# Kernel optimization log

Hardware: AMD Instinct MI355X
Metric: run time of the kernel (lower is better)

Reference implementation:

```python
import jax, jax.numpy as jnp
import numpy as np


def setup_inputs() -> dict:
    key = jax.random.key(0)
    ks = jax.random.split(key, 7)
    B, T, C, D = 8, 2048, 1024, 128
    x = jax.random.normal(ks[0], (B, T, C), dtype=jnp.float32)
    # torch nn.Linear weights are [out_features, in_features]
    s = 1.0 / np.sqrt(C)
    Wq = jax.random.normal(ks[1], (D, C), dtype=jnp.float32) * s
    bq = jax.random.normal(ks[2], (D,), dtype=jnp.float32) * s
    Wk = jax.random.normal(ks[3], (D, C), dtype=jnp.float32) * s
    bk = jax.random.normal(ks[4], (D,), dtype=jnp.float32) * s
    Wv = jax.random.normal(ks[5], (D, C), dtype=jnp.float32) * s
    bv = jax.random.normal(ks[6], (D,), dtype=jnp.float32) * s
    return {"x": x, "Wq": Wq, "bq": bq, "Wk": Wk, "bk": bk, "Wv": Wv, "bv": bv}


def reference(x, Wq, bq, Wk, bk, Wv, bv):
    B, T, C = x.shape
    q = jnp.einsum('btc,dc->btd', x, Wq) + bq  # [B,T,D]
    k = jnp.einsum('btc,dc->btd', x, Wk) + bk
    v = jnp.einsum('btc,dc->btd', x, Wv) + bv
    scores = jnp.einsum('btd,bsd->bts', q, k)  # [B,T,T]
    causal = jnp.tril(jnp.ones((T, T), dtype=bool))
    masked = jnp.where(causal, scores, -jnp.inf)
    # NOTE: original scales by sqrt(key.weight.shape[-1]) == sqrt(emb_dim), AFTER masking
    scale = jnp.asarray(C, dtype=x.dtype) ** 0.5
    attn = jax.nn.softmax(masked / scale, axis=-1)
    return jnp.einsum('bts,bsd->btd', attn, v)
```

## Files before the change

### kernel.cpp

```cpp
#include <hip/hip_runtime.h>
#include <hip/hip_bf16.h>
#include <math.h>

typedef __bf16 bf16_t;
typedef __bf16 bf16x4 __attribute__((ext_vector_type(4)));
typedef __bf16 bf16x8 __attribute__((ext_vector_type(8)));
typedef float  f32x4  __attribute__((ext_vector_type(4)));
typedef float  f32x16 __attribute__((ext_vector_type(16)));
typedef int    v2i    __attribute__((ext_vector_type(2)));

static constexpr int Bz = 8, Tt = 2048, Cc = 1024, Dd = 128;
static constexpr int Mm = Bz * Tt;
static constexpr int NT128 = Tt / 128;

__device__ __forceinline__ bf16x8 lds_read8(const char* base, int byte) {
    return *(const bf16x8*)(base + byte);
}

__device__ __forceinline__ bf16x8 cvt8(float4 a, float4 b) {
    bf16x8 r;
    r[0] = (bf16_t)a.x; r[1] = (bf16_t)a.y; r[2] = (bf16_t)a.z; r[3] = (bf16_t)a.w;
    r[4] = (bf16_t)b.x; r[5] = (bf16_t)b.y; r[6] = (bf16_t)b.z; r[7] = (bf16_t)b.w;
    return r;
}

__device__ __forceinline__ unsigned cvtpk(float lo, float hi) {
    unsigned r;
    asm("v_cvt_pk_bf16_f32 %0, %1, %2" : "=v"(r) : "v"(lo), "v"(hi));
    return r;
}

typedef const __attribute__((address_space(1))) unsigned int* as1_u32p;
typedef __attribute__((address_space(3))) unsigned int* as3_u32p;

__device__ __forceinline__ void gload_lds16(const bf16_t* g, bf16_t* l) {
    __builtin_amdgcn_global_load_lds((as1_u32p)(const void*)g, (as3_u32p)(void*)l, 16, 0, 0);
}

__global__ __launch_bounds__(256) void wcvt_kernel(
    const float* __restrict__ Wq, const float* __restrict__ Wk,
    const float* __restrict__ Wv, bf16_t* __restrict__ Wp)
{
    int g = (blockIdx.x * 256 + threadIdx.x) * 4;
    int n = g >> 10;
    int k = g & 1023;
    int sel = n >> 7;
    const float* W = (sel == 0) ? Wq : (sel == 1) ? Wk : Wv;
    float4 f = *(const float4*)(W + (size_t)(n & 127) * 1024 + k);
    bf16x4 o; o[0] = (bf16_t)f.x; o[1] = (bf16_t)f.y; o[2] = (bf16_t)f.z; o[3] = (bf16_t)f.w;
    int ktile = k >> 6, kk = (k >> 5) & 1, hi = (k >> 3) & 3, e = k & 7;
    int ng = n >> 4, cg = ng / 12, ngl = ng % 12, lo = n & 15;
    size_t addr = (size_t)(((((ktile * 2 + cg) * 12 + ngl) * 2 + kk) * 4 + hi) * 16 + lo) * 8 + e;
    *(bf16x4*)(Wp + addr) = o;
}

__global__ __launch_bounds__(512, 4) void qkv_fused(
    const float* __restrict__ x, const bf16_t* __restrict__ Wp,
    const float* __restrict__ bq, const float* __restrict__ bk, const float* __restrict__ bv,
    bf16_t* __restrict__ qo, bf16_t* __restrict__ ko, bf16_t* __restrict__ vTo)
{
    const int m0  = blockIdx.x * 64;
    const int cg  = blockIdx.y;
    const int tid = threadIdx.x;
    const int lane = tid & 63;
    const int wv  = tid >> 6;
    const int wr  = wv >> 2;
    const int cw  = wv & 3;
    const int lo  = lane & 15;
    const int hi  = lane >> 4;

    __shared__ bf16_t Wl[2][12 * 2 * 512];
    __shared__ bf16_t Xs[2][64 * 64];

    f32x4 zero4 = {0.f, 0.f, 0.f, 0.f};
    f32x4 acc[2][3];
    #pragma unroll
    for (int i = 0; i < 2; i++)
        #pragma unroll
        for (int j = 0; j < 3; j++) acc[i][j] = zero4;

    const int xrow = tid >> 3;
    const int xcol = (tid & 7) * 8;

    float4 fx[2];
    auto load_x = [&](int t) {
        const float4* s = (const float4*)(x + (size_t)(m0 + xrow) * Cc + t * 64 + xcol);
        fx[0] = s[0]; fx[1] = s[1];
    };
    auto write_x = [&](int buf) {
        int byte = (xrow * 128 + xcol * 2) ^ ((xrow & 7) << 4);
        *(bf16x8*)((char*)Xs[buf] + byte) = cvt8(fx[0], fx[1]);
    };
    auto stage_W = [&](int buf, int t) {
        const bf16_t* base = Wp + (size_t)(t * 2 + cg) * 12288;
        #pragma unroll
        for (int i = 0; i < 3; i++) {
            int c = i * 8 + wv;
            gload_lds16(base + c * 512 + lane * 8, Wl[buf] + c * 512);
        }
    };
    auto compute = [&](int buf) {
        #pragma unroll
        for (int kk = 0; kk < 2; kk++) {
            int r0 = wr * 32 + lo;
            int r1 = wr * 32 + 16 + lo;
            bf16x8 af0 = lds_read8((char*)Xs[buf], (r0 * 128 + kk * 64 + hi * 16) ^ ((r0 & 7) << 4));
            bf16x8 af1 = lds_read8((char*)Xs[buf], (r1 * 128 + kk * 64 + hi * 16) ^ ((r1 & 7) << 4));
            #pragma unroll
            for (int j = 0; j < 3; j++) {
                bf16x8 bf = *(const bf16x8*)(Wl[buf] + ((cw * 3 + j) * 2 + kk) * 512 + lane * 8);
                acc[0][j] = __builtin_amdgcn_mfma_f32_16x16x32_bf16(af0, bf, acc[0][j], 0, 0, 0);
                acc[1][j] = __builtin_amdgcn_mfma_f32_16x16x32_bf16(af1, bf, acc[1][j], 0, 0, 0);
            }
        }
    };

    load_x(0);
    stage_W(0, 0);
    write_x(0);
    load_x(1);
    asm volatile("s_waitcnt lgkmcnt(0)" ::: "memory");
    __builtin_amdgcn_s_barrier();

    #pragma unroll 1
    for (int t = 0; t < 16; t++) {
        const int buf = t & 1;
        if (t < 15) {
            stage_W(buf ^ 1, t + 1);
            asm volatile("s_waitcnt vmcnt(5)" ::: "memory");
        } else {
            asm volatile("s_waitcnt vmcnt(0)" ::: "memory");
        }
        __builtin_amdgcn_sched_barrier(0);
        compute(buf);
        if (t < 15) {
            write_x(buf ^ 1);
            if (t < 14) load_x(t + 2);
            asm volatile("s_waitcnt lgkmcnt(0)" ::: "memory");
            __builtin_amdgcn_s_barrier();
        }
    }

    #pragma unroll
    for (int j = 0; j < 3; j++) {
        int n = cg * 192 + cw * 48 + j * 16 + lo;
        int tsel = n >> 7, d = n & 127;
        const float* bp = (tsel == 0) ? bq : (tsel == 1) ? bk : bv;
        float bb = bp[d];
        #pragma unroll
        for (int i = 0; i < 2; i++)
            #pragma unroll
            for (int r = 0; r < 4; r++) {
                int m = m0 + wr * 32 + i * 16 + hi * 4 + r;
                float v = acc[i][j][r] + bb;
                if (tsel == 0)      qo[(size_t)m * Dd + d] = (bf16_t)v;
                else if (tsel == 1) ko[(size_t)m * Dd + d] = (bf16_t)v;
                else                vTo[(size_t)d * Mm + m] = (bf16_t)v;
            }
    }
}

__global__ __launch_bounds__(256, 2) void attn_kernel(
    const bf16_t* __restrict__ qi, const bf16_t* __restrict__ ki,
    const bf16_t* __restrict__ vTi,
    bf16_t* __restrict__ Opart, float* __restrict__ Mpart, float* __restrict__ Lpart,
    int nsplit)
{
    const int g   = blockIdx.x;
    const int per = nsplit * 8;
    const int qt  = (NT128 - 1) - g / per;
    const int rem = g % per;
    const int s   = rem >> 3;
    const int b   = rem & 7;
    const int nt  = 2 * qt + 2;
    const int t_lo = (s * nt) / nsplit;
    const int t_hi = ((s + 1) * nt) / nsplit;

    const int q0   = qt * 128;
    const int tid  = threadIdx.x;
    const int lane = tid & 63;
    const int w    = tid >> 6;
    const int rq   = lane & 31;
    const int dh   = lane >> 5;

    bf16_t* Ob = Opart + ((size_t)s * Mm + (size_t)b * Tt + q0) * Dd;
    float* Mb = Mpart + (size_t)s * Mm + (size_t)b * Tt + q0;
    float* Lb = Lpart + (size_t)s * Mm + (size_t)b * Tt + q0;

    if (t_lo >= t_hi) {
        float4 z = {0.f, 0.f, 0.f, 0.f};
        #pragma unroll
        for (int i = 0; i < 8; i++)
            ((float4*)Ob)[i * 256 + tid] = z;
        if (tid < 128) { Mb[tid] = -INFINITY; Lb[tid] = 0.f; }
        return;
    }

    __shared__ __align__(16) char smem[65536];

    const float SCALE = 1.4426950408889634f / 32.0f;
    const int qg = q0 + w * 32 + rq;
    const int qwmax = q0 + w * 32 + 31;

    bf16x8 qf[8];
    {
        const bf16_t* qrow = qi + (size_t)(b * Tt + qg) * Dd;
        #pragma unroll
        for (int ks = 0; ks < 8; ks++)
            qf[ks] = *(const bf16x8*)(qrow + ks * 16 + dh * 8);
    }

    f32x16 accO[4];
    #pragma unroll
    for (int ds = 0; ds < 4; ds++)
        #pragma unroll
        for (int e = 0; e < 16; e++) accO[ds][e] = 0.f;
    float mrun = -INFINITY, lrun = 0.f;

    const int krow = tid >> 2;
    const int kcol = (tid & 3) * 32;
    const int vrow = tid >> 1;
    const int vcol = (tid & 1) * 32;

    bf16x8 kr[4], vr[4];
    auto load_kv = [&](int t) {
        const int kv0 = t * 64;
        const bf16_t* ksrc = ki + (size_t)(b * Tt + kv0 + krow) * Dd + kcol;
        #pragma unroll
        for (int i = 0; i < 4; i++) kr[i] = *(const bf16x8*)(ksrc + i * 8);
        const bf16_t* vsrc = vTi + (size_t)vrow * Mm + (b * Tt + kv0 + vcol);
        #pragma unroll
        for (int i = 0; i < 4; i++) vr[i] = *(const bf16x8*)(vsrc + i * 8);
    };
    auto write_kv = [&](int buf) {
        char* Ksb = smem + buf * 16384;
        char* Vsb = smem + 32768 + buf * 16384;
        #pragma unroll
        for (int i = 0; i < 4; i++) {
            int byte = (krow * 256 + (kcol + i * 8) * 2) ^ ((krow & 15) << 4);
            *(bf16x8*)(Ksb + byte) = kr[i];
        }
        const int vlr = vrow & 63;
        const int vlc = (vrow >> 6) * 64 + vcol;
        #pragma unroll
        for (int i = 0; i < 4; i++) {
            int byte = (vlr * 256 + (vlc + i * 8) * 2) ^ ((vlr & 15) << 4);
            *(bf16x8*)(Vsb + byte) = vr[i];
        }
    };

    load_kv(t_lo);
    write_kv(0);
    int buf = 0;

    for (int t = t_lo; t < t_hi; t++) {
        const int kv0 = t * 64;
        const bool more = (t + 1 < t_hi);
        __syncthreads();
        if (more) load_kv(t + 1);

        if (kv0 <= qwmax) {
            const char* Ksb = smem + buf * 16384;
            const char* Vsb = smem + 32768 + buf * 16384;

            f32x16 accS0, accS1;
            #pragma unroll
            for (int e = 0; e < 16; e++) { accS0[e] = 0.f; accS1[e] = 0.f; }
            #pragma unroll
            for (int ks = 0; ks < 8; ks++) {
                int colb = (ks * 16 + dh * 8) * 2;
                bf16x8 kf0 = lds_read8(Ksb, ((rq)      * 256 + colb) ^ ((rq & 15) << 4));
                bf16x8 kf1 = lds_read8(Ksb, ((32 + rq) * 256 + colb) ^ ((rq & 15) << 4));
                accS0 = __builtin_amdgcn_mfma_f32_32x32x16_bf16(kf0, qf[ks], accS0, 0, 0, 0);
                accS1 = __builtin_amdgcn_mfma_f32_32x32x16_bf16(kf1, qf[ks], accS1, 0, 0, 0);
            }

            float pl[32];
            #pragma unroll
            for (int e = 0; e < 16; e++) {
                pl[e]      = accS0[e] * SCALE;
                pl[16 + e] = accS1[e] * SCALE;
            }
            if (kv0 + 63 > qg) {
                #pragma unroll
                for (int e = 0; e < 16; e++) {
                    int kg = kv0 + 8 * (e >> 2) + (e & 3) + 4 * dh;
                    if (kg > qg)      pl[e]      = -INFINITY;
                    if (kg + 32 > qg) pl[16 + e] = -INFINITY;
                }
            }

            float mt = pl[0];
            #pragma unroll
            for (int e = 1; e < 32; e++) mt = fmaxf(mt, pl[e]);
            mt = fmaxf(mt, __shfl_xor(mt, 32, 64));
            float mnew = fmaxf(mrun, mt);
            float muse = (mnew == -INFINITY) ? 0.f : mnew;
            float alpha = exp2f(mrun - muse);
            mrun = mnew;
            float ps = 0.f;
            #pragma unroll
            for (int e = 0; e < 32; e++) {
                float pv = exp2f(pl[e] - muse);
                pl[e] = pv;
                ps += pv;
            }
            lrun = alpha * lrun + ps;
            #pragma unroll
            for (int ds = 0; ds < 4; ds++)
                #pragma unroll
                for (int e = 0; e < 16; e++) accO[ds][e] *= alpha;

            unsigned u0[8], u1[8];
            #pragma unroll
            for (int gg = 0; gg < 8; gg++) {
                u0[gg] = cvtpk(pl[4 * gg + 0], pl[4 * gg + 1]);
                u1[gg] = cvtpk(pl[4 * gg + 2], pl[4 * gg + 3]);
            }
            bf16x8 pa[4];
            #pragma unroll
            for (int ks = 0; ks < 4; ks++) {
                v2i rA = __builtin_amdgcn_permlane32_swap((int)u0[2 * ks], (int)u0[2 * ks + 1], false, false);
                v2i rB = __builtin_amdgcn_permlane32_swap((int)u1[2 * ks], (int)u1[2 * ks + 1], false, false);
                union { unsigned wd[4]; bf16x8 v; } pu;
                pu.wd[0] = (unsigned)rA[0];
                pu.wd[1] = (unsigned)rB[0];
                pu.wd[2] = (unsigned)rA[1];
                pu.wd[3] = (unsigned)rB[1];
                pa[ks] = pu.v;
            }

            #pragma unroll
            for (int ds = 0; ds < 4; ds++) {
                int row  = (ds & 1) * 32 + rq;
                int cb   = (ds >> 1) * 64;
                #pragma unroll
                for (int ks = 0; ks < 4; ks++) {
                    int colb = (cb + ks * 16 + dh * 8) * 2;
                    bf16x8 vf = lds_read8(Vsb, (row * 256 + colb) ^ ((row & 15) << 4));
                    accO[ds] = __builtin_amdgcn_mfma_f32_32x32x16_bf16(vf, pa[ks], accO[ds], 0, 0, 0);
                }
            }
        }

        __syncthreads();
        if (more) write_kv(buf ^ 1);
        buf ^= 1;
    }

    __syncthreads();

    lrun += __shfl_xor(lrun, 32, 64);

    char* slab = smem + w * 8192;
    #pragma unroll
    for (int half = 0; half < 2; half++) {
        #pragma unroll
        for (int dsl = 0; dsl < 2; dsl++) {
            #pragma unroll
            for (int e = 0; e < 16; e++) {
                int d = 8 * (e >> 2) + (e & 3) + 4 * dh + 32 * dsl;
                int byte = (rq * 256 + d * 4) ^ ((rq & 15) << 4);
                *(float*)(slab + byte) = accO[half * 2 + dsl][e];
            }
        }
        __builtin_amdgcn_s_waitcnt(0);
        #pragma unroll
        for (int i = 0; i < 8; i++) {
            int dd = 32 * dh + 4 * i;
            int byte = (rq * 256 + dd * 4) ^ ((rq & 15) << 4);
            float4 val = *(float4*)(slab + byte);
            bf16x4 o; o[0] = (bf16_t)val.x; o[1] = (bf16_t)val.y;
            o[2] = (bf16_t)val.z; o[3] = (bf16_t)val.w;
            *(bf16x4*)(Ob + (size_t)(w * 32 + rq) * Dd + half * 64 + dd) = o;
        }
        __builtin_amdgcn_s_waitcnt(0);
    }

    if (lane < 32) {
        Mb[w * 32 + rq] = mrun;
        Lb[w * 32 + rq] = lrun;
    }
}

__global__ __launch_bounds__(256) void combine_kernel(
    const bf16_t* __restrict__ Opart, const float* __restrict__ Mpart,
    const float* __restrict__ Lpart, float* __restrict__ out, int nsplit)
{
    int t   = blockIdx.x * 256 + threadIdx.x;
    int row = t >> 5;
    int dq  = (t & 31) << 2;
    float M = -INFINITY;
    for (int s = 0; s < nsplit; s++)
        M = fmaxf(M, Mpart[(size_t)s * Mm + row]);
    float L = 0.f;
    float o0 = 0.f, o1 = 0.f, o2 = 0.f, o3 = 0.f;
    for (int s = 0; s < nsplit; s++) {
        float ms = Mpart[(size_t)s * Mm + row];
        float ws = (ms == -INFINITY) ? 0.f : exp2f(ms - M);
        L += ws * Lpart[(size_t)s * Mm + row];
        bf16x4 p = *(const bf16x4*)(Opart + ((size_t)s * Mm + row) * Dd + dq);
        o0 += ws * (float)p[0]; o1 += ws * (float)p[1];
        o2 += ws * (float)p[2]; o3 += ws * (float)p[3];
    }
    float inv = 1.0f / L;
    float4 r; r.x = o0 * inv; r.y = o1 * inv; r.z = o2 * inv; r.w = o3 * inv;
    *(float4*)(out + (size_t)row * Dd + dq) = r;
}

extern "C" void kernel_launch(void* const* d_in, const int* in_sizes, int n_in,
                              void* d_out, int out_size, void* d_ws, size_t ws_size,
                              hipStream_t stream)
{
    const float* x  = (const float*)d_in[0];
    const float* Wq = (const float*)d_in[1];
    const float* bq = (const float*)d_in[2];
    const float* Wk = (const float*)d_in[3];
    const float* bk = (const float*)d_in[4];
    const float* Wv = (const float*)d_in[5];
    const float* bv = (const float*)d_in[6];
    float* out = (float*)d_out;

    bf16_t* qb = (bf16_t*)d_ws;
    bf16_t* kb = qb + (size_t)Mm * Dd;
    bf16_t* vT = kb + (size_t)Mm * Dd;
    bf16_t* Wp = vT + (size_t)Mm * Dd;
    char* p = (char*)(Wp + (size_t)384 * Cc);

    auto need = [&](int ns) {
        return (size_t)3 * Mm * Dd * 2 + (size_t)384 * Cc * 2
             + (size_t)ns * Mm * Dd * 2 + (size_t)ns * Mm * 8;
    };
    int nsplit = 4;
    while (nsplit > 1 && need(nsplit) > ws_size) nsplit >>= 1;

    bf16_t* Opart = (bf16_t*)p;
    float* Mpart = (float*)(p + (size_t)nsplit * Mm * Dd * 2);
    float* Lpart = Mpart + (size_t)nsplit * Mm;

    wcvt_kernel<<<dim3(384), 256, 0, stream>>>(Wq, Wk, Wv, Wp);
    qkv_fused<<<dim3(256, 2), 512, 0, stream>>>(x, Wp, bq, bk, bv, qb, kb, vT);
    attn_kernel<<<dim3(NT128 * nsplit * Bz), 256, 0, stream>>>(qb, kb, vT, Opart, Mpart, Lpart, nsplit);
    combine_kernel<<<dim3(Mm * 32 / 256), 256, 0, stream>>>(Opart, Mpart, Lpart, out, nsplit);
}
```

Before: 64.65 us.

## Fuse split-KV combine into attention kernel via last-block atomic counter

The separate combine kernel is removed. Each attention block now increments a per-(query tile, batch) atomic counter, and the last split to finish merges all partial outputs into the final result. Empty splits no longer zero their Opart slab and the merge simply skips them. This saves a kernel launch and some Opart traffic, at the cost of a memset launch, thread fences, and a serialized combine tail in the last block of each tile.

```diff
diff --git a/kernel.cpp b/kernel.cpp
--- a/kernel.cpp
+++ b/kernel.cpp
@@ -164,7 +164,7 @@
     const bf16_t* __restrict__ qi, const bf16_t* __restrict__ ki,
     const bf16_t* __restrict__ vTi,
     bf16_t* __restrict__ Opart, float* __restrict__ Mpart, float* __restrict__ Lpart,
-    int nsplit)
+    unsigned* __restrict__ counters, float* __restrict__ out, int nsplit)
 {
     const int g   = blockIdx.x;
     const int per = nsplit * 8;
@@ -187,225 +187,228 @@
     float* Mb = Mpart + (size_t)s * Mm + (size_t)b * Tt + q0;
     float* Lb = Lpart + (size_t)s * Mm + (size_t)b * Tt + q0;
 
-    if (t_lo >= t_hi) {
-        float4 z = {0.f, 0.f, 0.f, 0.f};
-        #pragma unroll
-        for (int i = 0; i < 8; i++)
-            ((float4*)Ob)[i * 256 + tid] = z;
-        if (tid < 128) { Mb[tid] = -INFINITY; Lb[tid] = 0.f; }
-        return;
-    }
-
     __shared__ __align__(16) char smem[65536];
+    __shared__ unsigned tick;
 
     const float SCALE = 1.4426950408889634f / 32.0f;
     const int qg = q0 + w * 32 + rq;
     const int qwmax = q0 + w * 32 + 31;
 
-    bf16x8 qf[8];
-    {
-        const bf16_t* qrow = qi + (size_t)(b * Tt + qg) * Dd;
-        #pragma unroll
-        for (int ks = 0; ks < 8; ks++)
-            qf[ks] = *(const bf16x8*)(qrow + ks * 16 + dh * 8);
+    if (t_lo < t_hi) {
+        bf16x8 qf[8];
+        {
+            const bf16_t* qrow = qi + (size_t)(b * Tt + qg) * Dd;
+            #pragma unroll
+            for (int ks = 0; ks < 8; ks++)
+                qf[ks] = *(const bf16x8*)(qrow + ks * 16 + dh * 8);
+        }
+
+        f32x16 accO[4];
+        #pragma unroll
+        for (int ds = 0; ds < 4; ds++)
+            #pragma unroll
+            for (int e = 0; e < 16; e++) accO[ds][e] = 0.f;
+        float mrun = -INFINITY, lrun = 0.f;
+
+        const int krow = tid >> 2;
+        const int kcol = (tid & 3) * 32;
+        const int vrow = tid >> 1;
+        const int vcol = (tid & 1) * 32;
+
+        bf16x8 kr[4], vr[4];
+        auto load_kv = [&](int t) {
+            const int kv0 = t * 64;
+            const bf16_t* ksrc = ki + (size_t)(b * Tt + kv0 + krow) * Dd + kcol;
+            #pragma unroll
+            for (int i = 0; i < 4; i++) kr[i] = *(const bf16x8*)(ksrc + i * 8);
+            const bf16_t* vsrc = vTi + (size_t)vrow * Mm + (b * Tt + kv0 + vcol);
+            #pragma unroll
+            for (int i = 0; i < 4; i++) vr[i] = *(const bf16x8*)(vsrc + i * 8);
+        };
+        auto write_kv = [&](int buf) {
+            char* Ksb = smem + buf * 16384;
+            char* Vsb = smem + 32768 + buf * 16384;
+            #pragma unroll
+            for (int i = 0; i < 4; i++) {
+                int byte = (krow * 256 + (kcol + i * 8) * 2) ^ ((krow & 15) << 4);
+                *(bf16x8*)(Ksb + byte) = kr[i];
+            }
+            const int vlr = vrow & 63;
+            const int vlc = (vrow >> 6) * 64 + vcol;
+            #pragma unroll
+            for (int i = 0; i < 4; i++) {
+                int byte = (vlr * 256 + (vlc + i * 8) * 2) ^ ((vlr & 15) << 4);
+                *(bf16x8*)(Vsb + byte) = vr[i];
+            }
+        };
+
+        load_kv(t_lo);
+        write_kv(0);
+        int buf = 0;
+
+        for (int t = t_lo; t < t_hi; t++) {
+            const int kv0 = t * 64;
+            const bool more = (t + 1 < t_hi);
+            __syncthreads();
+            if (more) load_kv(t + 1);
+
+            if (kv0 <= qwmax) {
+                const char* Ksb = smem + buf * 16384;
+                const char* Vsb = smem + 32768 + buf * 16384;
+
+                f32x16 accS0, accS1;
+                #pragma unroll
+                for (int e = 0; e < 16; e++) { accS0[e] = 0.f; accS1[e] = 0.f; }
+                #pragma unroll
+                for (int ks = 0; ks < 8; ks++) {
+                    int colb = (ks * 16 + dh * 8) * 2;
+                    bf16x8 kf0 = lds_read8(Ksb, ((rq)      * 256 + colb) ^ ((rq & 15) << 4));
+                    bf16x8 kf1 = lds_read8(Ksb, ((32 + rq) * 256 + colb) ^ ((rq & 15) << 4));
+                    accS0 = __builtin_amdgcn_mfma_f32_32x32x16_bf16(kf0, qf[ks], accS0, 0, 0, 0);
+                    accS1 = __builtin_amdgcn_mfma_f32_32x32x16_bf16(kf1, qf[ks], accS1, 0, 0, 0);
+                }
+
+                float pl[32];
+                #pragma unroll
+                for (int e = 0; e < 16; e++) {
+                    pl[e]      = accS0[e] * SCALE;
+                    pl[16 + e] = accS1[e] * SCALE;
+                }
+                if (kv0 + 63 > qg) {
+                    #pragma unroll
+                    for (int e = 0; e < 16; e++) {
+                        int kg = kv0 + 8 * (e >> 2) + (e & 3) + 4 * dh;
+                        if (kg > qg)      pl[e]      = -INFINITY;
+                        if (kg + 32 > qg) pl[16 + e] = -INFINITY;
+                    }
+                }
+
+                float mt = pl[0];
+                #pragma unroll
+                for (int e = 1; e < 32; e++) mt = fmaxf(mt, pl[e]);
+                mt = fmaxf(mt, __shfl_xor(mt, 32, 64));
+                float mnew = fmaxf(mrun, mt);
+                float muse = (mnew == -INFINITY) ? 0.f : mnew;
+                float alpha = exp2f(mrun - muse);
+                mrun = mnew;
+                float ps = 0.f;
+                #pragma unroll
+                for (int e = 0; e < 32; e++) {
+                    float pv = exp2f(pl[e] - muse);
+                    pl[e] = pv;
+                    ps += pv;
+                }
+                lrun = alpha * lrun + ps;
+                #pragma unroll
+                for (int ds = 0; ds < 4; ds++)
+                    #pragma unroll
+                    for (int e = 0; e < 16; e++) accO[ds][e] *= alpha;
+
+                unsigned u0[8], u1[8];
+                #pragma unroll
+                for (int gg = 0; gg < 8; gg++) {
+                    u0[gg] = cvtpk(pl[4 * gg + 0], pl[4 * gg + 1]);
+                    u1[gg] = cvtpk(pl[4 * gg + 2], pl[4 * gg + 3]);
+                }
+                bf16x8 pa[4];
+                #pragma unroll
+                for (int ks = 0; ks < 4; ks++) {
+                    v2i rA = __builtin_amdgcn_permlane32_swap((int)u0[2 * ks], (int)u0[2 * ks + 1], false, false);
+                    v2i rB = __builtin_amdgcn_permlane32_swap((int)u1[2 * ks], (int)u1[2 * ks + 1], false, false);
+                    union { unsigned wd[4]; bf16x8 v; } pu;
+                    pu.wd[0] = (unsigned)rA[0];
+                    pu.wd[1] = (unsigned)rB[0];
+                    pu.wd[2] = (unsigned)rA[1];
+                    pu.wd[3] = (unsigned)rB[1];
+                    pa[ks] = pu.v;
+                }
+
+                #pragma unroll
+                for (int ds = 0; ds < 4; ds++) {
+                    int row  = (ds & 1) * 32 + rq;
+                    int cb   = (ds >> 1) * 64;
+                    #pragma unroll
+                    for (int ks = 0; ks < 4; ks++) {
+                        int colb = (cb + ks * 16 + dh * 8) * 2;
+                        bf16x8 vf = lds_read8(Vsb, (row * 256 + colb) ^ ((row & 15) << 4));
+                        accO[ds] = __builtin_amdgcn_mfma_f32_32x32x16_bf16(vf, pa[ks], accO[ds], 0, 0, 0);
+                    }
+                }
+            }
+
+            __syncthreads();
+            if (more) write_kv(buf ^ 1);
+            buf ^= 1;
+        }
+
+        __syncthreads();
+
+        lrun += __shfl_xor(lrun, 32, 64);
+
+        char* slab = smem + w * 8192;
+        #pragma unroll
+        for (int half = 0; half < 2; half++) {
+            #pragma unroll
+            for (int dsl = 0; dsl < 2; dsl++) {
+                #pragma unroll
+                for (int e = 0; e < 16; e++) {
+                    int d = 8 * (e >> 2) + (e & 3) + 4 * dh + 32 * dsl;
+                    int byte = (rq * 256 + d * 4) ^ ((rq & 15) << 4);
+                    *(float*)(slab + byte) = accO[half * 2 + dsl][e];
+                }
+            }
+            __builtin_amdgcn_s_waitcnt(0);
+            #pragma unroll
+            for (int i = 0; i < 8; i++) {
+                int dd = 32 * dh + 4 * i;
+                int byte = (rq * 256 + dd * 4) ^ ((rq & 15) << 4);
+                float4 val = *(float4*)(slab + byte);
+                bf16x4 o; o[0] = (bf16_t)val.x; o[1] = (bf16_t)val.y;
+                o[2] = (bf16_t)val.z; o[3] = (bf16_t)val.w;
+                *(bf16x4*)(Ob + (size_t)(w * 32 + rq) * Dd + half * 64 + dd) = o;
+            }
+            __builtin_amdgcn_s_waitcnt(0);
+        }
+
+        if (lane < 32) {
+            Mb[w * 32 + rq] = mrun;
+            Lb[w * 32 + rq] = lrun;
+        }
+    } else {
+        if (tid < 128) { Mb[tid] = -INFINITY; Lb[tid] = 0.f; }
     }
 
-    f32x16 accO[4];
-    #pragma unroll
-    for (int ds = 0; ds < 4; ds++)
-        #pragma unroll
-        for (int e = 0; e < 16; e++) accO[ds][e] = 0.f;
-    float mrun = -INFINITY, lrun = 0.f;
-
-    const int krow = tid >> 2;
-    const int kcol = (tid & 3) * 32;
-    const int vrow = tid >> 1;
-    const int vcol = (tid & 1) * 32;
-
-    bf16x8 kr[4], vr[4];
-    auto load_kv = [&](int t) {
-        const int kv0 = t * 64;
-        const bf16_t* ksrc = ki + (size_t)(b * Tt + kv0 + krow) * Dd + kcol;
-        #pragma unroll
-        for (int i = 0; i < 4; i++) kr[i] = *(const bf16x8*)(ksrc + i * 8);
-        const bf16_t* vsrc = vTi + (size_t)vrow * Mm + (b * Tt + kv0 + vcol);
-        #pragma unroll
-        for (int i = 0; i < 4; i++) vr[i] = *(const bf16x8*)(vsrc + i * 8);
-    };
-    auto write_kv = [&](int buf) {
-        char* Ksb = smem + buf * 16384;
-        char* Vsb = smem + 32768 + buf * 16384;
-        #pragma unroll
-        for (int i = 0; i < 4; i++) {
-            int byte = (krow * 256 + (kcol + i * 8) * 2) ^ ((krow & 15) << 4);
-            *(bf16x8*)(Ksb + byte) = kr[i];
-        }
-        const int vlr = vrow & 63;
-        const int vlc = (vrow >> 6) * 64 + vcol;
-        #pragma unroll
-        for (int i = 0; i < 4; i++) {
-            int byte = (vlr * 256 + (vlc + i * 8) * 2) ^ ((vlr & 15) << 4);
-            *(bf16x8*)(Vsb + byte) = vr[i];
-        }
-    };
-
-    load_kv(t_lo);
-    write_kv(0);
-    int buf = 0;
-
-    for (int t = t_lo; t < t_hi; t++) {
-        const int kv0 = t * 64;
-        const bool more = (t + 1 < t_hi);
-        __syncthreads();
-        if (more) load_kv(t + 1);
-
-        if (kv0 <= qwmax) {
-            const char* Ksb = smem + buf * 16384;
-            const char* Vsb = smem + 32768 + buf * 16384;
-
-            f32x16 accS0, accS1;
-            #pragma unroll
-            for (int e = 0; e < 16; e++) { accS0[e] = 0.f; accS1[e] = 0.f; }
-            #pragma unroll
-            for (int ks = 0; ks < 8; ks++) {
-                int colb = (ks * 16 + dh * 8) * 2;
-                bf16x8 kf0 = lds_read8(Ksb, ((rq)      * 256 + colb) ^ ((rq & 15) << 4));
-                bf16x8 kf1 = lds_read8(Ksb, ((32 + rq) * 256 + colb) ^ ((rq & 15) << 4));
-                accS0 = __builtin_amdgcn_mfma_f32_32x32x16_bf16(kf0, qf[ks], accS0, 0, 0, 0);
-                accS1 = __builtin_amdgcn_mfma_f32_32x32x16_bf16(kf1, qf[ks], accS1, 0, 0, 0);
-            }
-
-            float pl[32];
-            #pragma unroll
-            for (int e = 0; e < 16; e++) {
-                pl[e]      = accS0[e] * SCALE;
-                pl[16 + e] = accS1[e] * SCALE;
-            }
-            if (kv0 + 63 > qg) {
-                #pragma unroll
-                for (int e = 0; e < 16; e++) {
-                    int kg = kv0 + 8 * (e >> 2) + (e & 3) + 4 * dh;
-                    if (kg > qg)      pl[e]      = -INFINITY;
-                    if (kg + 32 > qg) pl[16 + e] = -INFINITY;
-                }
-            }
-
-            float mt = pl[0];
-            #pragma unroll
-            for (int e = 1; e < 32; e++) mt = fmaxf(mt, pl[e]);
-            mt = fmaxf(mt, __shfl_xor(mt, 32, 64));
-            float mnew = fmaxf(mrun, mt);
-            float muse = (mnew == -INFINITY) ? 0.f : mnew;
-            float alpha = exp2f(mrun - muse);
-            mrun = mnew;
-            float ps = 0.f;
-            #pragma unroll
-            for (int e = 0; e < 32; e++) {
-                float pv = exp2f(pl[e] - muse);
-                pl[e] = pv;
-                ps += pv;
-            }
-            lrun = alpha * lrun + ps;
-            #pragma unroll
-            for (int ds = 0; ds < 4; ds++)
-                #pragma unroll
-                for (int e = 0; e < 16; e++) accO[ds][e] *= alpha;
-
-            unsigned u0[8], u1[8];
-            #pragma unroll
-            for (int gg = 0; gg < 8; gg++) {
-                u0[gg] = cvtpk(pl[4 * gg + 0], pl[4 * gg + 1]);
-                u1[gg] = cvtpk(pl[4 * gg + 2], pl[4 * gg + 3]);
-            }
-            bf16x8 pa[4];
-            #pragma unroll
-            for (int ks = 0; ks < 4; ks++) {
-                v2i rA = __builtin_amdgcn_permlane32_swap((int)u0[2 * ks], (int)u0[2 * ks + 1], false, false);
-                v2i rB = __builtin_amdgcn_permlane32_swap((int)u1[2 * ks], (int)u1[2 * ks + 1], false, false);
-                union { unsigned wd[4]; bf16x8 v; } pu;
-                pu.wd[0] = (unsigned)rA[0];
-                pu.wd[1] = (unsigned)rB[0];
-                pu.wd[2] = (unsigned)rA[1];
-                pu.wd[3] = (unsigned)rB[1];
-                pa[ks] = pu.v;
-            }
-
-            #pragma unroll
-            for (int ds = 0; ds < 4; ds++) {
-                int row  = (ds & 1) * 32 + rq;
-                int cb   = (ds >> 1) * 64;
-                #pragma unroll
-                for (int ks = 0; ks < 4; ks++) {
-                    int colb = (cb + ks * 16 + dh * 8) * 2;
-                    bf16x8 vf = lds_read8(Vsb, (row * 256 + colb) ^ ((row & 15) << 4));
-                    accO[ds] = __builtin_amdgcn_mfma_f32_32x32x16_bf16(vf, pa[ks], accO[ds], 0, 0, 0);
-                }
-            }
-        }
-
-        __syncthreads();
-        if (more) write_kv(buf ^ 1);
-        buf ^= 1;
+    __threadfence();
+    __syncthreads();
+    if (tid == 0) tick = atomicAdd(&counters[qt * 8 + b], 1u);
+    __syncthreads();
+    if (tick != (unsigned)(nsplit - 1)) return;
+    __threadfence();
+
+    #pragma unroll 1
+    for (int i = 0; i < 16; i++) {
+        int idx = i * 256 + tid;
+        int rr  = idx >> 5;
+        int dq  = (idx & 31) << 2;
+        size_t rowg = (size_t)b * Tt + q0 + rr;
+        float M = -INFINITY;
+        for (int s2 = 0; s2 < nsplit; s2++)
+            M = fmaxf(M, Mpart[(size_t)s2 * Mm + rowg]);
+        float L = 0.f;
+        float o0 = 0.f, o1 = 0.f, o2 = 0.f, o3 = 0.f;
+        for (int s2 = 0; s2 < nsplit; s2++) {
+            float ms = Mpart[(size_t)s2 * Mm + rowg];
+            if (ms == -INFINITY) continue;
+            float ws = exp2f(ms - M);
+            L += ws * Lpart[(size_t)s2 * Mm + rowg];
+            bf16x4 pv = *(const bf16x4*)(Opart + ((size_t)s2 * Mm + rowg) * Dd + dq);
+            o0 += ws * (float)pv[0]; o1 += ws * (float)pv[1];
+            o2 += ws * (float)pv[2]; o3 += ws * (float)pv[3];
+        }
+        float inv = 1.0f / L;
+        float4 r; r.x = o0 * inv; r.y = o1 * inv; r.z = o2 * inv; r.w = o3 * inv;
+        *(float4*)(out + rowg * Dd + dq) = r;
     }
-
-    __syncthreads();
-
-    lrun += __shfl_xor(lrun, 32, 64);
-
-    char* slab = smem + w * 8192;
-    #pragma unroll
-    for (int half = 0; half < 2; half++) {
-        #pragma unroll
-        for (int dsl = 0; dsl < 2; dsl++) {
-            #pragma unroll
-            for (int e = 0; e < 16; e++) {
-                int d = 8 * (e >> 2) + (e & 3) + 4 * dh + 32 * dsl;
-                int byte = (rq * 256 + d * 4) ^ ((rq & 15) << 4);
-                *(float*)(slab + byte) = accO[half * 2 + dsl][e];
-            }
-        }
-        __builtin_amdgcn_s_waitcnt(0);
-        #pragma unroll
-        for (int i = 0; i < 8; i++) {
-            int dd = 32 * dh + 4 * i;
-            int byte = (rq * 256 + dd * 4) ^ ((rq & 15) << 4);
-            float4 val = *(float4*)(slab + byte);
-            bf16x4 o; o[0] = (bf16_t)val.x; o[1] = (bf16_t)val.y;
-            o[2] = (bf16_t)val.z; o[3] = (bf16_t)val.w;
-            *(bf16x4*)(Ob + (size_t)(w * 32 + rq) * Dd + half * 64 + dd) = o;
-        }
-        __builtin_amdgcn_s_waitcnt(0);
-    }
-
-    if (lane < 32) {
-        Mb[w * 32 + rq] = mrun;
-        Lb[w * 32 + rq] = lrun;
-    }
-}
-
-__global__ __launch_bounds__(256) void combine_kernel(
-    const bf16_t* __restrict__ Opart, const float* __restrict__ Mpart,
-    const float* __restrict__ Lpart, float* __restrict__ out, int nsplit)
-{
-    int t   = blockIdx.x * 256 + threadIdx.x;
-    int row = t >> 5;
-    int dq  = (t & 31) << 2;
-    float M = -INFINITY;
-    for (int s = 0; s < nsplit; s++)
-        M = fmaxf(M, Mpart[(size_t)s * Mm + row]);
-    float L = 0.f;
-    float o0 = 0.f, o1 = 0.f, o2 = 0.f, o3 = 0.f;
-    for (int s = 0; s < nsplit; s++) {
-        float ms = Mpart[(size_t)s * Mm + row];
-        float ws = (ms == -INFINITY) ? 0.f : exp2f(ms - M);
-        L += ws * Lpart[(size_t)s * Mm + row];
-        bf16x4 p = *(const bf16x4*)(Opart + ((size_t)s * Mm + row) * Dd + dq);
-        o0 += ws * (float)p[0]; o1 += ws * (float)p[1];
-        o2 += ws * (float)p[2]; o3 += ws * (float)p[3];
-    }
-    float inv = 1.0f / L;
-    float4 r; r.x = o0 * inv; r.y = o1 * inv; r.z = o2 * inv; r.w = o3 * inv;
-    *(float4*)(out + (size_t)row * Dd + dq) = r;
 }
 
 extern "C" void kernel_launch(void* const* d_in, const int* in_sizes, int n_in,
@@ -429,7 +432,7 @@
 
     auto need = [&](int ns) {
         return (size_t)3 * Mm * Dd * 2 + (size_t)384 * Cc * 2
-             + (size_t)ns * Mm * Dd * 2 + (size_t)ns * Mm * 8;
+             + (size_t)ns * Mm * Dd * 2 + (size_t)ns * Mm * 8 + 512;
     };
     int nsplit = 4;
     while (nsplit > 1 && need(nsplit) > ws_size) nsplit >>= 1;
@@ -437,9 +440,10 @@
     bf16_t* Opart = (bf16_t*)p;
     float* Mpart = (float*)(p + (size_t)nsplit * Mm * Dd * 2);
     float* Lpart = Mpart + (size_t)nsplit * Mm;
-
+    unsigned* counters = (unsigned*)(Lpart + (size_t)nsplit * Mm);
+
+    hipMemsetAsync(counters, 0, 128 * sizeof(unsigned), stream);
     wcvt_kernel<<<dim3(384), 256, 0, stream>>>(Wq, Wk, Wv, Wp);
     qkv_fused<<<dim3(256, 2), 512, 0, stream>>>(x, Wp, bq, bk, bv, qb, kb, vT);
-    attn_kernel<<<dim3(NT128 * nsplit * Bz), 256, 0, stream>>>(qb, kb, vT, Opart, Mpart, Lpart, nsplit);
-    combine_kernel<<<dim3(Mm * 32 / 256), 256, 0, stream>>>(Opart, Mpart, Lpart, out, nsplit);
-}
+    attn_kernel<<<dim3(NT128 * nsplit * Bz), 256, 0, stream>>>(qb, kb, vT, Opart, Mpart, Lpart, counters, out, nsplit);
+}
```

Measured after the change: 189.8 us. +193.5%, slower.
